# Kernel optimization log

Measured on AMD Instinct MI355X. Metric: run time of the kernel, lower is better.

The kernel has to match this reference:

```python
import jax, jax.numpy as jnp
import numpy as np

N, D, DIM, H = 50000, 32, 128, 4  # nodes, fixed degree, feature dim, heads


def setup_inputs() -> dict:
    key = jax.random.key(0)
    ks = jax.random.split(key, 8)
    s = 1.0 / np.sqrt(DIM)
    h = jax.random.normal(ks[0], (N, DIM), dtype=jnp.float32)
    neigh_idx = jax.random.randint(ks[1], (N, D), 0, N, dtype=jnp.int32)
    W = jax.random.uniform(ks[2], (H, DIM, DIM), jnp.float32, -s, s)   # per-head fciandj
    a1 = jax.random.uniform(ks[3], (H, DIM), jnp.float32, -s, s)       # key weight, src half
    a2 = jax.random.uniform(ks[4], (H, DIM), jnp.float32, -s, s)       # key weight, nbr half
    Wg = jax.random.uniform(ks[5], (DIM, H), jnp.float32, -s, s)       # GetGate projection
    W0 = jax.random.uniform(ks[6], (H * DIM, DIM), jnp.float32, -s, s) # output mix w0
    return {"h": h, "neigh_idx": neigh_idx, "W": W, "a1": a1, "a2": a2, "Wg": Wg, "W0": W0}


def reference(h, neigh_idx, W, a1, a2, Wg, W0):
    # gate per node per head (GetGate assumed: softmax over heads of linear proj)
    g = jax.nn.softmax(h @ Wg, axis=-1)            # [N, H]
    hjs = h[neigh_idx]                              # [N, D, d] per-edge gather (shared across heads)
    heads = []
    for k in range(W.shape[0]):
        wh = h @ W[k]                               # [N, d]
        whjs = jnp.einsum('ndi,ij->ndj', hjs, W[k]) # [N, D, d]
        # edge score: key([wh_i, wh_j]) = wh_i.a1 + wh_j.a2, then leaky_relu
        e = jax.nn.leaky_relu((wh @ a1[k])[:, None] + whjs @ a2[k])  # [N, D]
        att = jax.nn.softmax(e, axis=1)             # segment softmax over neighbors
        out = jax.nn.relu(jnp.einsum('nd,ndj->nj', att, whjs))       # [N, d]
        heads.append(g[:, k:k + 1] * out)
    return jnp.concatenate(heads, axis=-1) @ W0     # [N, d]
```

## Files before the change

### kernel.cpp

```cpp
#include <hip/hip_runtime.h>

typedef __attribute__((ext_vector_type(8))) short short8;
typedef __attribute__((ext_vector_type(4))) float f32x4;
typedef __attribute__((ext_vector_type(2))) float f32x2;

__device__ __forceinline__ float bf2f(unsigned u16) {
    union { float f; unsigned u32; } v; v.u32 = u16 << 16; return v.f;
}
__device__ __forceinline__ unsigned short f2bf(float f) {
    union { float f; unsigned u32; } v; v.f = f;
    unsigned x = v.u32;
    x += ((x >> 16) & 1u) + 0x7FFFu;
    return (unsigned short)(x >> 16);
}
__device__ __forceinline__ unsigned packbf(float a, float b) {
    return (unsigned)f2bf(a) | ((unsigned)f2bf(b) << 16);
}
__device__ __forceinline__ f32x2 unpack2(unsigned hv) {
    union { float f; unsigned u; } lo, hi;
    lo.u = hv << 16;
    hi.u = hv & 0xffff0000u;
    f32x2 r; r.x = lo.f; r.y = hi.f; return r;
}

__global__ __launch_bounds__(256) void kb12(const float* __restrict__ W,
                                            const float* __restrict__ a1,
                                            const float* __restrict__ a2,
                                            float* __restrict__ b1,
                                            float* __restrict__ b2) {
    int idx = blockIdx.x * 256 + threadIdx.x;
    int k = idx >> 7, i = idx & 127;
    const float* wr = &W[k * 16384 + i * 128];
    const float* A1 = &a1[k * 128];
    const float* A2 = &a2[k * 128];
    float v1 = 0.f, v2 = 0.f;
    for (int c = 0; c < 128; ++c) { float wv = wr[c]; v1 += wv * A1[c]; v2 += wv * A2[c]; }
    b1[k * 128 + i] = v1;
    b2[k * 128 + i] = v2;
}

__global__ __launch_bounds__(256) void kscore(const float* __restrict__ h,
                                              const float* __restrict__ Wg,
                                              const float* __restrict__ b1,
                                              const float* __restrict__ b2,
                                              unsigned* __restrict__ hb32,
                                              float* __restrict__ s1,
                                              float* __restrict__ s2,
                                              float* __restrict__ g,
                                              int N) {
    const int t = threadIdx.x, w = t >> 6, l = t & 63;
    const int grp = l >> 4, q = l & 15;
    const int n = blockIdx.x * 16 + w * 4 + grp;
    if (n >= N) return;

    float4 hv0 = *(const float4*)&h[(size_t)n * 128 + q * 8];
    float4 hv1 = *(const float4*)&h[(size_t)n * 128 + q * 8 + 4];
    float ha[8] = {hv0.x, hv0.y, hv0.z, hv0.w, hv1.x, hv1.y, hv1.z, hv1.w};

    uint4 hbv;
    hbv.x = packbf(ha[0], ha[1]); hbv.y = packbf(ha[2], ha[3]);
    hbv.z = packbf(ha[4], ha[5]); hbv.w = packbf(ha[6], ha[7]);
    *(uint4*)&hb32[(size_t)n * 64 + q * 4] = hbv;

    float p[12];
    #pragma unroll
    for (int k = 0; k < 4; ++k) {
        float4 ba = *(const float4*)&b1[k * 128 + q * 8];
        float4 bb = *(const float4*)&b1[k * 128 + q * 8 + 4];
        p[k] = ha[0]*ba.x + ha[1]*ba.y + ha[2]*ba.z + ha[3]*ba.w
             + ha[4]*bb.x + ha[5]*bb.y + ha[6]*bb.z + ha[7]*bb.w;
        float4 ca = *(const float4*)&b2[k * 128 + q * 8];
        float4 cb = *(const float4*)&b2[k * 128 + q * 8 + 4];
        p[4+k] = ha[0]*ca.x + ha[1]*ca.y + ha[2]*ca.z + ha[3]*ca.w
               + ha[4]*cb.x + ha[5]*cb.y + ha[6]*cb.z + ha[7]*cb.w;
    }
    p[8] = p[9] = p[10] = p[11] = 0.f;
    #pragma unroll
    for (int e = 0; e < 8; ++e) {
        float4 wg = *(const float4*)&Wg[(q * 8 + e) * 4];
        p[8]  += ha[e] * wg.x;
        p[9]  += ha[e] * wg.y;
        p[10] += ha[e] * wg.z;
        p[11] += ha[e] * wg.w;
    }
    #pragma unroll
    for (int m = 8; m >= 1; m >>= 1) {
        #pragma unroll
        for (int i = 0; i < 12; ++i) p[i] += __shfl_xor(p[i], m, 16);
    }
    if (q == 0) {
        *(float4*)&s1[n * 4] = make_float4(p[0], p[1], p[2], p[3]);
        *(float4*)&s2[n * 4] = make_float4(p[4], p[5], p[6], p[7]);
        float mx = fmaxf(fmaxf(p[8], p[9]), fmaxf(p[10], p[11]));
        float e0 = __expf(p[8] - mx), e1 = __expf(p[9] - mx);
        float e2 = __expf(p[10] - mx), e3 = __expf(p[11] - mx);
        float si = 1.f / (e0 + e1 + e2 + e3);
        *(float4*)&g[n * 4] = make_float4(e0 * si, e1 * si, e2 * si, e3 * si);
    }
}

__global__ __launch_bounds__(512) void k3_mix(const int* __restrict__ idx,
                                              const unsigned* __restrict__ hb32,
                                              const float* __restrict__ s1,
                                              const float* __restrict__ s2,
                                              unsigned* __restrict__ Mx32,
                                              const float* __restrict__ W,
                                              const float* __restrict__ W0,
                                              unsigned short* __restrict__ Wt,
                                              unsigned short* __restrict__ W0t,
                                              int N, int nb) {
    const int b = blockIdx.x, tid = threadIdx.x;
    if (b >= nb) {
        int bb = b - nb;
        if (bb < 128) {
            int i = bb * 512 + tid;
            int head = i >> 14, rem = i & 16383, k = rem >> 7, col = rem & 127;
            Wt[head * 16384 + col * 128 + k] = f2bf(W[i]);
        } else {
            int i = (bb - 128) * 512 + tid;
            int k = i >> 7, col = i & 127;
            W0t[col * 512 + k] = f2bf(W0[i]);
        }
        return;
    }

    __shared__ float att4s[8][32][4];
    const int w = tid >> 6, l = tid & 63;
    const int d = l & 31, half = l >> 5;
    int n = b * 8 + w;
    const bool valid = (n < N);
    if (!valid) n = N - 1;

    int j = idx[(size_t)n * 32 + d];
    float2 s2v = *(const float2*)&s2[(size_t)j * 4 + half * 2];
    const float* s1p = &s1[(size_t)n * 4];
    float e0 = s1p[half * 2] + s2v.x;
    float e1 = s1p[half * 2 + 1] + s2v.y;
    e0 = (e0 >= 0.f) ? e0 : 0.01f * e0;
    e1 = (e1 >= 0.f) ? e1 : 0.01f * e1;
    float m0 = e0, m1 = e1;
    #pragma unroll
    for (int mm = 16; mm >= 1; mm >>= 1) {
        m0 = fmaxf(m0, __shfl_xor(m0, mm, 32));
        m1 = fmaxf(m1, __shfl_xor(m1, mm, 32));
    }
    float p0 = __expf(e0 - m0), p1 = __expf(e1 - m1);
    float q0 = p0, q1 = p1;
    #pragma unroll
    for (int mm = 16; mm >= 1; mm >>= 1) {
        q0 += __shfl_xor(q0, mm, 32);
        q1 += __shfl_xor(q1, mm, 32);
    }
    *(float2*)&att4s[w][d][half * 2] = make_float2(p0 / q0, p1 / q1);

    f32x2 ac0 = {}, ac1 = {}, ac2 = {}, ac3 = {};
    #pragma unroll
    for (int dd = 0; dd < 32; ++dd) {
        int jj = __shfl(j, dd, 64);
        unsigned hv = hb32[(size_t)jj * 64 + l];
        f32x2 h01 = unpack2(hv);
        float4 a4 = *(const float4*)&att4s[w][dd][0];
        ac0 += (f32x2){a4.x, a4.x} * h01;
        ac1 += (f32x2){a4.y, a4.y} * h01;
        ac2 += (f32x2){a4.z, a4.z} * h01;
        ac3 += (f32x2){a4.w, a4.w} * h01;
    }
    if (valid) {
        Mx32[(size_t)n * 256 +   0 + l] = packbf(ac0.x, ac0.y);
        Mx32[(size_t)n * 256 +  64 + l] = packbf(ac1.x, ac1.y);
        Mx32[(size_t)n * 256 + 128 + l] = packbf(ac2.x, ac2.y);
        Mx32[(size_t)n * 256 + 192 + l] = packbf(ac3.x, ac3.y);
    }
}

typedef const __attribute__((address_space(1))) char gbyte;
typedef __attribute__((address_space(3))) char lbyte;

__global__ __launch_bounds__(512, 1) void k4_gemm(const unsigned short* __restrict__ Mx,
                                                  const unsigned short* __restrict__ Wt,
                                                  const unsigned short* __restrict__ W0t,
                                                  const float* __restrict__ g,
                                                  float* __restrict__ out,
                                                  int N, int T) {
    __shared__ unsigned short Uin[32 * 512];
    __shared__ unsigned short Uout[32 * 512];
    __shared__ float gld[128];
    const int tid = threadIdx.x, w = tid >> 6, l = tid & 63;
    const int l15 = l & 15, lh = l >> 4;
    const int hd = w & 3, ch = w >> 2;
    const int P = gridDim.x;

    short8 bf1[4][4];
    #pragma unroll
    for (int s = 0; s < 4; ++s)
        #pragma unroll
        for (int c = 0; c < 4; ++c)
            bf1[s][c] = *(const short8*)&Wt[(size_t)hd * 16384 +
                                            (size_t)((ch * 4 + c) * 16 + l15) * 128 + s * 32 + lh * 8];
    short8 bf2[16];
    #pragma unroll
    for (int ks = 0; ks < 16; ++ks)
        bf2[ks] = *(const short8*)&W0t[(size_t)(w * 16 + l15) * 512 + ks * 32 + lh * 8];

    const int t0 = blockIdx.x;

    auto STAGE = [&](int tile) {
        const size_t n0 = (size_t)tile * 32;
        if (w == 0 && l < 32) {
            size_t n = n0 + l; if (n >= (size_t)N) n = N - 1;
            __builtin_amdgcn_global_load_lds((gbyte*)((const char*)g + n * 16),
                                             (lbyte*)&gld[0], 16, 0, 0);
        }
        #pragma unroll
        for (int p = 0; p < 4; ++p) {
            int r = p * 8 + w;
            size_t n = n0 + r;
            if (n >= (size_t)N) n = N - 1;
            const char* src = (const char*)Mx + n * 1024 + ((l * 16) ^ ((r & 7) << 4));
            __builtin_amdgcn_global_load_lds((gbyte*)src, (lbyte*)&Uin[r * 512], 16, 0, 0);
        }
    };

    STAGE(t0);
    __syncthreads();

    for (int t = t0; t < T; t += P) {
        const int n0 = t * 32;

        const char* Uib = (const char*)Uin;
        #pragma unroll
        for (int rg = 0; rg < 2; ++rg) {
            const int arow = rg * 16 + l15;
            short8 af[4];
            #pragma unroll
            for (int s = 0; s < 4; ++s) {
                int ab = arow * 1024 + hd * 256 + s * 64 + lh * 16;
                af[s] = *(const short8*)(Uib + (ab ^ ((arow & 7) << 4)));
            }
            f32x4 acc[4] = {};
            #pragma unroll
            for (int s = 0; s < 4; ++s)
                #pragma unroll
                for (int c = 0; c < 4; ++c)
                    acc[c] = __builtin_amdgcn_mfma_f32_16x16x32_bf16(af[s], bf1[s][c], acc[c], 0, 0, 0);
            #pragma unroll
            for (int c = 0; c < 4; ++c) {
                const int col = hd * 128 + (ch * 4 + c) * 16 + l15;
                #pragma unroll
                for (int r = 0; r < 4; ++r) {
                    int row = rg * 16 + lh * 4 + r;
                    float v = fmaxf(acc[c][r], 0.f) * gld[row * 4 + hd];
                    int ub = row * 1024 + col * 2;
                    *(unsigned short*)((char*)Uout + (ub ^ ((row & 7) << 4))) = f2bf(v);
                }
            }
        }

        __syncthreads();

        if (t + P < T) STAGE(t + P);

        const char* Uob = (const char*)Uout;
        #pragma unroll
        for (int rg = 0; rg < 2; ++rg) {
            const int arow = rg * 16 + l15;
            f32x4 oacc = {};
            #pragma unroll
            for (int ks = 0; ks < 16; ++ks) {
                int ab = arow * 1024 + ks * 64 + lh * 16;
                short8 afr = *(const short8*)(Uob + (ab ^ ((arow & 7) << 4)));
                oacc = __builtin_amdgcn_mfma_f32_16x16x32_bf16(afr, bf2[ks], oacc, 0, 0, 0);
            }
            #pragma unroll
            for (int r = 0; r < 4; ++r) {
                int n = n0 + rg * 16 + lh * 4 + r;
                if (n < N) out[(size_t)n * 128 + w * 16 + l15] = oacc[r];
            }
        }

        __syncthreads();
    }
}

extern "C" void kernel_launch(void* const* d_in, const int* in_sizes, int n_in,
                              void* d_out, int out_size, void* d_ws, size_t ws_size,
                              hipStream_t stream) {
    const float* h     = (const float*)d_in[0];
    const int*   neigh = (const int*)d_in[1];
    const float* W     = (const float*)d_in[2];
    const float* a1    = (const float*)d_in[3];
    const float* a2    = (const float*)d_in[4];
    const float* Wg    = (const float*)d_in[5];
    const float* W0    = (const float*)d_in[6];
    float* out = (float*)d_out;

    const int N = in_sizes[0] / 128;

    char* ws = (char*)d_ws;
    unsigned* hb32 = (unsigned*)ws;
    unsigned* Mx32 = (unsigned*)(ws + (size_t)N * 256);
    float* s1 = (float*)(ws + (size_t)N * 256 + (size_t)N * 1024);
    float* s2 = s1 + (size_t)N * 4;
    float* g  = s2 + (size_t)N * 4;
    unsigned short* Wt  = (unsigned short*)(g + (size_t)N * 4);
    unsigned short* W0t = Wt + 65536;
    float* b1 = (float*)(W0t + 65536);
    float* b2 = b1 + 512;

    const int nb = (N + 7) / 8;
    const int T = (N + 31) / 32;
    const int P = (T < 256) ? T : 256;

    kb12<<<dim3(2), dim3(256), 0, stream>>>(W, a1, a2, b1, b2);
    kscore<<<dim3((N + 15) / 16), dim3(256), 0, stream>>>(h, Wg, b1, b2, hb32, s1, s2, g, N);
    k3_mix<<<dim3(nb + 256), dim3(512), 0, stream>>>(neigh, hb32, s1, s2, Mx32,
                                                     W, W0, Wt, W0t, N, nb);
    k4_gemm<<<dim3(P), dim3(512), 0, stream>>>((const unsigned short*)Mx32, Wt, W0t, g,
                                               out, N, T);
}
```

Baseline: 123.5 us.

## Move weight transposes into score kernel, shrink mix blocks, split MFMA accumulators

The W/W0 bf16 transpose work moves from the gather/mix kernel into extra blocks of the score kernel. The mix kernel is cut to 256-thread blocks covering 4 nodes each, and its packed-float2 accumulation becomes scalar accumulation. The output GEMM now alternates two independent MFMA accumulators to break the dependency chain. Together these aim to improve scheduling and latency hiding, at the cost of more launched blocks and a possible loss of packed-FMA throughput.

```diff
diff --git a/kernel.cpp b/kernel.cpp
--- a/kernel.cpp
+++ b/kernel.cpp
@@ -2,7 +2,6 @@
 
 typedef __attribute__((ext_vector_type(8))) short short8;
 typedef __attribute__((ext_vector_type(4))) float f32x4;
-typedef __attribute__((ext_vector_type(2))) float f32x2;
 
 __device__ __forceinline__ float bf2f(unsigned u16) {
     union { float f; unsigned u32; } v; v.u32 = u16 << 16; return v.f;
@@ -15,12 +14,6 @@
 }
 __device__ __forceinline__ unsigned packbf(float a, float b) {
     return (unsigned)f2bf(a) | ((unsigned)f2bf(b) << 16);
-}
-__device__ __forceinline__ f32x2 unpack2(unsigned hv) {
-    union { float f; unsigned u; } lo, hi;
-    lo.u = hv << 16;
-    hi.u = hv & 0xffff0000u;
-    f32x2 r; r.x = lo.f; r.y = hi.f; return r;
 }
 
 __global__ __launch_bounds__(256) void kb12(const float* __restrict__ W,
@@ -43,14 +36,34 @@
                                               const float* __restrict__ Wg,
                                               const float* __restrict__ b1,
                                               const float* __restrict__ b2,
+                                              const float* __restrict__ W,
+                                              const float* __restrict__ W0,
                                               unsigned* __restrict__ hb32,
                                               float* __restrict__ s1,
                                               float* __restrict__ s2,
                                               float* __restrict__ g,
+                                              unsigned short* __restrict__ Wt,
+                                              unsigned short* __restrict__ W0t,
                                               int N) {
-    const int t = threadIdx.x, w = t >> 6, l = t & 63;
+    const int b = blockIdx.x, t = threadIdx.x;
+    if (b < 256) {
+        #pragma unroll
+        for (int e = 0; e < 2; ++e) {
+            int i = b * 512 + e * 256 + t;
+            if (i < 65536) {
+                int head = i >> 14, rem = i & 16383, k = rem >> 7, col = rem & 127;
+                Wt[head * 16384 + col * 128 + k] = f2bf(W[i]);
+            } else {
+                int i2 = i - 65536;
+                int k = i2 >> 7, col = i2 & 127;
+                W0t[col * 512 + k] = f2bf(W0[i2]);
+            }
+        }
+        return;
+    }
+    const int w = t >> 6, l = t & 63;
     const int grp = l >> 4, q = l & 15;
-    const int n = blockIdx.x * 16 + w * 4 + grp;
+    const int n = (b - 256) * 16 + w * 4 + grp;
     if (n >= N) return;
 
     float4 hv0 = *(const float4*)&h[(size_t)n * 128 + q * 8];
@@ -99,35 +112,16 @@
     }
 }
 
-__global__ __launch_bounds__(512) void k3_mix(const int* __restrict__ idx,
+__global__ __launch_bounds__(256) void k3_mix(const int* __restrict__ idx,
                                               const unsigned* __restrict__ hb32,
                                               const float* __restrict__ s1,
                                               const float* __restrict__ s2,
                                               unsigned* __restrict__ Mx32,
-                                              const float* __restrict__ W,
-                                              const float* __restrict__ W0,
-                                              unsigned short* __restrict__ Wt,
-                                              unsigned short* __restrict__ W0t,
-                                              int N, int nb) {
-    const int b = blockIdx.x, tid = threadIdx.x;
-    if (b >= nb) {
-        int bb = b - nb;
-        if (bb < 128) {
-            int i = bb * 512 + tid;
-            int head = i >> 14, rem = i & 16383, k = rem >> 7, col = rem & 127;
-            Wt[head * 16384 + col * 128 + k] = f2bf(W[i]);
-        } else {
-            int i = (bb - 128) * 512 + tid;
-            int k = i >> 7, col = i & 127;
-            W0t[col * 512 + k] = f2bf(W0[i]);
-        }
-        return;
-    }
-
-    __shared__ float att4s[8][32][4];
-    const int w = tid >> 6, l = tid & 63;
+                                              int N) {
+    __shared__ float att4s[4][32][4];
+    const int t = threadIdx.x, w = t >> 6, l = t & 63;
     const int d = l & 31, half = l >> 5;
-    int n = b * 8 + w;
+    int n = blockIdx.x * 4 + w;
     const bool valid = (n < N);
     if (!valid) n = N - 1;
 
@@ -153,23 +147,23 @@
     }
     *(float2*)&att4s[w][d][half * 2] = make_float2(p0 / q0, p1 / q1);
 
-    f32x2 ac0 = {}, ac1 = {}, ac2 = {}, ac3 = {};
+    float ac[4][2] = {};
     #pragma unroll
     for (int dd = 0; dd < 32; ++dd) {
         int jj = __shfl(j, dd, 64);
         unsigned hv = hb32[(size_t)jj * 64 + l];
-        f32x2 h01 = unpack2(hv);
+        float h0 = bf2f(hv & 0xffffu);
+        float h1 = bf2f(hv >> 16);
         float4 a4 = *(const float4*)&att4s[w][dd][0];
-        ac0 += (f32x2){a4.x, a4.x} * h01;
-        ac1 += (f32x2){a4.y, a4.y} * h01;
-        ac2 += (f32x2){a4.z, a4.z} * h01;
-        ac3 += (f32x2){a4.w, a4.w} * h01;
+        ac[0][0] += a4.x * h0; ac[0][1] += a4.x * h1;
+        ac[1][0] += a4.y * h0; ac[1][1] += a4.y * h1;
+        ac[2][0] += a4.z * h0; ac[2][1] += a4.z * h1;
+        ac[3][0] += a4.w * h0; ac[3][1] += a4.w * h1;
     }
     if (valid) {
-        Mx32[(size_t)n * 256 +   0 + l] = packbf(ac0.x, ac0.y);
-        Mx32[(size_t)n * 256 +  64 + l] = packbf(ac1.x, ac1.y);
-        Mx32[(size_t)n * 256 + 128 + l] = packbf(ac2.x, ac2.y);
-        Mx32[(size_t)n * 256 + 192 + l] = packbf(ac3.x, ac3.y);
+        #pragma unroll
+        for (int k = 0; k < 4; ++k)
+            Mx32[(size_t)n * 256 + k * 64 + l] = packbf(ac[k][0], ac[k][1]);
     }
 }
 
@@ -264,13 +258,17 @@
         #pragma unroll
         for (int rg = 0; rg < 2; ++rg) {
             const int arow = rg * 16 + l15;
-            f32x4 oacc = {};
-            #pragma unroll
-            for (int ks = 0; ks < 16; ++ks) {
-                int ab = arow * 1024 + ks * 64 + lh * 16;
-                short8 afr = *(const short8*)(Uob + (ab ^ ((arow & 7) << 4)));
-                oacc = __builtin_amdgcn_mfma_f32_16x16x32_bf16(afr, bf2[ks], oacc, 0, 0, 0);
-            }
+            f32x4 oaccA = {}, oaccB = {};
+            #pragma unroll
+            for (int ks = 0; ks < 16; ks += 2) {
+                int abA = arow * 1024 + ks * 64 + lh * 16;
+                int abB = abA + 64;
+                short8 afrA = *(const short8*)(Uob + (abA ^ ((arow & 7) << 4)));
+                short8 afrB = *(const short8*)(Uob + (abB ^ ((arow & 7) << 4)));
+                oaccA = __builtin_amdgcn_mfma_f32_16x16x32_bf16(afrA, bf2[ks], oaccA, 0, 0, 0);
+                oaccB = __builtin_amdgcn_mfma_f32_16x16x32_bf16(afrB, bf2[ks + 1], oaccB, 0, 0, 0);
+            }
+            f32x4 oacc = oaccA + oaccB;
             #pragma unroll
             for (int r = 0; r < 4; ++r) {
                 int n = n0 + rg * 16 + lh * 4 + r;
@@ -307,14 +305,13 @@
     float* b1 = (float*)(W0t + 65536);
     float* b2 = b1 + 512;
 
-    const int nb = (N + 7) / 8;
     const int T = (N + 31) / 32;
     const int P = (T < 256) ? T : 256;
 
     kb12<<<dim3(2), dim3(256), 0, stream>>>(W, a1, a2, b1, b2);
-    kscore<<<dim3((N + 15) / 16), dim3(256), 0, stream>>>(h, Wg, b1, b2, hb32, s1, s2, g, N);
-    k3_mix<<<dim3(nb + 256), dim3(512), 0, stream>>>(neigh, hb32, s1, s2, Mx32,
-                                                     W, W0, Wt, W0t, N, nb);
+    kscore<<<dim3((N + 15) / 16 + 256), dim3(256), 0, stream>>>(h, Wg, b1, b2, W, W0,
+                                                                hb32, s1, s2, g, Wt, W0t, N);
+    k3_mix<<<dim3((N + 3) / 4), dim3(256), 0, stream>>>(neigh, hb32, s1, s2, Mx32, N);
     k4_gemm<<<dim3(P), dim3(512), 0, stream>>>((const unsigned short*)Mx32, Wt, W0t, g,
                                                out, N, T);
 }
```

Measured after the change: 120.4 us. 2.5% less time.
